# Optimization experiments

Hardware: AMD Instinct MI355X
Metric: run time of the kernel (lower is better)

Reference implementation:

```python
import jax, jax.numpy as jnp
import numpy as np

# NOTE: the original source omits the definitions of QSVT, quantum_lcu_block,
# QuantumSumBlock and KANLayer. We reconstruct the standard math these blocks
# implement in quantum-KAN papers/repos:
#   QSVT(x)            -> vector of Chebyshev polynomials T_1..T_D of the
#                         (squashed) input, the polynomial basis QSVT realizes.
#   quantum_lcu_block  -> linear combination of unitaries: weighted sum of the
#                         QSVT vector normalized by the LCU l1 weight norm.
#   QuantumSumBlock    -> learnable interference sum: mean_k sin(alpha_k * v).
#   KANLayer           -> Chebyshev-KAN layer: spline term (Chebyshev basis
#                         contracted with coeffs) + SiLU base branch + bias.
# Everything is fully vectorized over (B, F) instead of the original per-scalar
# Python loops.

B, F, DEG, C, KBASIS = 16384, 512, 8, 10, 8


def _cheb(x, K):
    """Chebyshev features T_1..T_K of x in (-1, 1): shape x.shape + (K,)."""
    t = jnp.arccos(jnp.clip(x, -1.0, 1.0))
    k = jnp.arange(1, K + 1, dtype=x.dtype)
    return jnp.cos(t[..., None] * k)


def setup_inputs() -> dict:
    key = jax.random.key(0)
    ks = jax.random.split(key, 6)
    return {
        "X": jax.random.normal(ks[0], (B, F), dtype=jnp.float32),
        # nn.Parameter(torch.rand(num_features, degree))
        "lcu_weights": jax.random.uniform(ks[1], (F, DEG), dtype=jnp.float32),
        # one QuantumSumBlock(degree) per feature -> (F, DEG) phases
        "sum_alpha": jax.random.normal(ks[2], (F, DEG), dtype=jnp.float32),
        # KANLayer params
        "kan_coeff": jax.random.normal(ks[3], (C, F, KBASIS), dtype=jnp.float32) * 0.1,
        "kan_base": jax.random.normal(ks[4], (C, F), dtype=jnp.float32) * 0.1,
        "kan_bias": jnp.zeros((C,), dtype=jnp.float32),
    }


def reference(X, lcu_weights, sum_alpha, kan_coeff, kan_base, kan_bias):
    # squash inputs into the open interval (-1, 1) for the Chebyshev/QSVT basis
    x = 0.99 * jnp.tanh(X)                                   # (B, F)
    # QSVT polynomial feature vector per scalar, batched: (B, F, DEG)
    qsvt = _cheb(x, lcu_weights.shape[1])
    # LCU block: weighted combination normalized by l1 norm of weights -> (B, F)
    lcu = jnp.einsum('bfd,fd->bf', qsvt, lcu_weights) / (
        jnp.sum(jnp.abs(lcu_weights), axis=-1) + 1e-8)
    # Quantum sum block: learnable sinusoidal interference sum -> (B, F)
    summed = jnp.mean(jnp.sin(lcu[..., None] * sum_alpha), axis=-1)
    # Chebyshev-KAN layer
    s = 0.99 * jnp.tanh(summed)
    phi = _cheb(s, kan_coeff.shape[2])                       # (B, F, KBASIS)
    logits = (jnp.einsum('bfk,cfk->bc', phi, kan_coeff)
              + jax.nn.silu(summed) @ kan_base.T
              + kan_bias)                                    # (B, C)
    return logits
```

## Files before the change

kernel.cpp:

```cpp
#include <hip/hip_runtime.h>
#include <hip/hip_bf16.h>

#define BATCH 16384
#define NF    512
#define DEG   8
#define NC    10
#define KB    8

#define RB     16
#define PITCH2 520
#define NT     512
#define NWAVES 8

#define CBN (NC * NF * KB)
#define BBN (NC * NF)

#define INV2PI 0.15915494309189535f
#define LOG2E  1.4426950408889634f

typedef __attribute__((ext_vector_type(2))) float v2f;
typedef __attribute__((ext_vector_type(8))) short bfrag;
typedef __attribute__((ext_vector_type(8))) unsigned short us8;
typedef __attribute__((ext_vector_type(4))) float f32x4;

union frag_u { bfrag s; unsigned u[4]; };

__device__ __forceinline__ v2f v2fma(v2f a, v2f b, v2f c) {
    return __builtin_elementwise_fma(a, b, c);
}
__device__ __forceinline__ v2f v2exp(v2f x) {
    v2f a = x * LOG2E;
    v2f r; r.x = __builtin_amdgcn_exp2f(a.x); r.y = __builtin_amdgcn_exp2f(a.y);
    return r;
}
__device__ __forceinline__ v2f v2rcp(v2f x) {
    v2f r; r.x = __builtin_amdgcn_rcpf(x.x); r.y = __builtin_amdgcn_rcpf(x.y);
    return r;
}
__device__ __forceinline__ v2f v2sin2pi(v2f x) {
    v2f r; r.x = __builtin_amdgcn_sinf(x.x); r.y = __builtin_amdgcn_sinf(x.y);
    return r;
}
__device__ __forceinline__ v2f v2tanh99(v2f x) {
    v2f e = v2exp(x + x);
    v2f r = v2rcp(e + 1.0f);
    return v2fma(r, (v2f)(-1.98f), (v2f)(0.99f));
}
__device__ __forceinline__ v2f v2silu(v2f v) {
    v2f e = v2exp(-v);
    v2f r = v2rcp(e + 1.0f);
    return v * r;
}
__device__ __forceinline__ unsigned cvtpk2(float lo, float hi) {
    __hip_bfloat162 h = __float22bfloat162_rn(float2{lo, hi});
    unsigned u;
    __builtin_memcpy(&u, &h, sizeof(u));
    return u;
}
__device__ __forceinline__ float bf2f(unsigned short h) {
    unsigned u = ((unsigned)h) << 16;
    return __builtin_bit_cast(float, u);
}

__global__ __launch_bounds__(256) void prep_kernel(
    const float* __restrict__ coeff, const float* __restrict__ base,
    unsigned short* __restrict__ pk)
{
    const int i = blockIdx.x * 256 + threadIdx.x;
    if (i < CBN)
        pk[i] = (unsigned short)((__builtin_bit_cast(unsigned, coeff[i]) + 0x8000u) >> 16);
    else if (i < CBN + BBN)
        pk[i] = (unsigned short)((__builtin_bit_cast(unsigned, base[i - CBN]) + 0x8000u) >> 16);
}

__global__ __launch_bounds__(NT, 8) void qkan_kernel(
    const float* __restrict__ X,
    const float* __restrict__ lcu_w,
    const float* __restrict__ alpha,
    const unsigned short* __restrict__ pk,
    const float* __restrict__ bias,
    float* __restrict__ out)
{
    __shared__ unsigned short s_mem[RB * PITCH2];
    __shared__ float s_red[NWAVES * RB * 16];

    const int t    = threadIdx.x;
    const int row0 = blockIdx.x * RB;

    {
        const int fA = (t & 255) * 2;
        const int rh = (t >> 8) * 8;

        float wa[2][DEG], aa[2][DEG], den[2];
#pragma unroll
        for (int i = 0; i < 2; ++i) {
            const float4 w0 = *(const float4*)(lcu_w + (fA + i) * DEG);
            const float4 w1 = *(const float4*)(lcu_w + (fA + i) * DEG + 4);
            const float4 a0 = *(const float4*)(alpha + (fA + i) * DEG);
            const float4 a1 = *(const float4*)(alpha + (fA + i) * DEG + 4);
            wa[i][0]=w0.x; wa[i][1]=w0.y; wa[i][2]=w0.z; wa[i][3]=w0.w;
            wa[i][4]=w1.x; wa[i][5]=w1.y; wa[i][6]=w1.z; wa[i][7]=w1.w;
            aa[i][0]=a0.x; aa[i][1]=a0.y; aa[i][2]=a0.z; aa[i][3]=a0.w;
            aa[i][4]=a1.x; aa[i][5]=a1.y; aa[i][6]=a1.z; aa[i][7]=a1.w;
            float d = 1e-8f;
#pragma unroll
            for (int k = 0; k < DEG; ++k) d += fabsf(wa[i][k]);
            den[i] = d;
        }
        v2f W[DEG], A2[DEG];
#pragma unroll
        for (int d = 0; d < DEG; ++d) {
            W[d]  = (v2f){wa[0][d], wa[1][d]};
            A2[d] = (v2f){aa[0][d] * INV2PI, aa[1][d] * INV2PI};
        }
        const v2f rden = (v2f){__builtin_amdgcn_rcpf(den[0]),
                               __builtin_amdgcn_rcpf(den[1])};

#pragma unroll 4
        for (int r8 = 0; r8 < 8; ++r8) {
            const int r = rh + r8;
            const v2f xv = *(const v2f*)(X + (row0 + r) * NF + fA);
            const v2f x  = v2tanh99(xv);
            const v2f x2 = x + x;
            v2f tkm1 = (v2f){1.0f, 1.0f}, tk = x, num = (v2f){0.0f, 0.0f};
#pragma unroll
            for (int d = 0; d < DEG; ++d) {
                num = v2fma(W[d], tk, num);
                v2f tn = v2fma(x2, tk, -tkm1);
                tkm1 = tk; tk = tn;
            }
            const v2f lcu = num * rden;
            v2f ss = (v2f){0.0f, 0.0f};
#pragma unroll
            for (int d = 0; d < DEG; ++d)
                ss += v2sin2pi(lcu * A2[d]);
            const v2f sm = ss * 0.125f;
            *(unsigned*)(&s_mem[r * PITCH2 + fA]) = cvtpk2(sm.x, sm.y);
        }
    }
    __syncthreads();

    const int lane = t & 63;
    const int wave = __builtin_amdgcn_readfirstlane(t >> 6);
    const int n    = lane & 15;
    const int q    = lane >> 4;
    const int ncl  = (n < NC) ? n : (NC - 1);
    const int fw   = wave * 64;

    const unsigned short* cb = pk;
    const unsigned short* bb = pk + CBN;
    const unsigned short* cbase = cb + (ncl * NF + fw) * KB;

    f32x4 acc0 = {0.f, 0.f, 0.f, 0.f};
    f32x4 acc1 = {0.f, 0.f, 0.f, 0.f};

#pragma unroll 4
    for (int kp = 0; kp < 8; ++kp) {
        const bfrag b0 = *(const bfrag*)(cbase + (kp * 8 + q) * KB);
        const bfrag b1 = *(const bfrag*)(cbase + (kp * 8 + 4 + q) * KB);

        const float sA = bf2f(s_mem[n * PITCH2 + fw + kp * 8 + q]);
        const float sB = bf2f(s_mem[n * PITCH2 + fw + kp * 8 + 4 + q]);
        const v2f s  = v2tanh99((v2f){sA, sB});
        const v2f s2 = s + s;
        v2f T[KB];
        {
            v2f tkm1 = (v2f){1.0f, 1.0f}, tk = s;
#pragma unroll
            for (int k = 0; k < KB; ++k) {
                T[k] = tk;
                v2f tn = v2fma(s2, tk, -tkm1);
                tkm1 = tk; tk = tn;
            }
        }
        frag_u fa0, fa1;
#pragma unroll
        for (int i = 0; i < 4; ++i) {
            fa0.u[i] = cvtpk2(T[2 * i].x, T[2 * i + 1].x);
            fa1.u[i] = cvtpk2(T[2 * i].y, T[2 * i + 1].y);
        }
        acc0 = __builtin_amdgcn_mfma_f32_16x16x32_bf16(fa0.s, b0, acc0, 0, 0, 0);
        acc1 = __builtin_amdgcn_mfma_f32_16x16x32_bf16(fa1.s, b1, acc1, 0, 0, 0);
    }

#pragma unroll
    for (int kt2 = 0; kt2 < 2; ++kt2) {
        const bfrag b = *(const bfrag*)(bb + ncl * NF + fw + kt2 * 32 + q * 8);
        const us8 sv = *(const us8*)(&s_mem[n * PITCH2 + fw + kt2 * 32 + q * 8]);
        v2f vv[4];
#pragma unroll
        for (int g = 0; g < 4; ++g)
            vv[g] = (v2f){bf2f(sv[2 * g]), bf2f(sv[2 * g + 1])};
        frag_u fa;
#pragma unroll
        for (int g = 0; g < 4; ++g) {
            const v2f sl = v2silu(vv[g]);
            fa.u[g] = cvtpk2(sl.x, sl.y);
        }
        if (kt2 & 1)
            acc1 = __builtin_amdgcn_mfma_f32_16x16x32_bf16(fa.s, b, acc1, 0, 0, 0);
        else
            acc0 = __builtin_amdgcn_mfma_f32_16x16x32_bf16(fa.s, b, acc0, 0, 0, 0);
    }

    const f32x4 acc = acc0 + acc1;
#pragma unroll
    for (int i = 0; i < 4; ++i)
        s_red[wave * (RB * 16) + (q * 4 + i) * 16 + n] = acc[i];
    __syncthreads();

    if (t < RB * NC) {
        const int r = t / NC;
        const int c = t - r * NC;
        float v = bias[c];
#pragma unroll
        for (int w = 0; w < NWAVES; ++w)
            v += s_red[w * (RB * 16) + r * 16 + c];
        out[(row0 + r) * NC + c] = v;
    }
}

extern "C" void kernel_launch(void* const* d_in, const int* in_sizes, int n_in,
                              void* d_out, int out_size, void* d_ws, size_t ws_size,
                              hipStream_t stream) {
    const float* X      = (const float*)d_in[0];
    const float* lcu_w  = (const float*)d_in[1];
    const float* alpha  = (const float*)d_in[2];
    const float* coeff  = (const float*)d_in[3];
    const float* base   = (const float*)d_in[4];
    const float* bias   = (const float*)d_in[5];
    float* out = (float*)d_out;
    unsigned short* pk = (unsigned short*)d_ws;

    prep_kernel<<<(CBN + BBN + 255) / 256, 256, 0, stream>>>(coeff, base, pk);
    qkan_kernel<<<BATCH / RB, NT, 0, stream>>>(X, lcu_w, alpha, pk, bias, out);
}
```

Before: 101.6 us.

## Compute tanh and SiLU in the first stage and halve block threads

After: 100.9 us. About the same (-0.7%).

```diff
diff --git a/kernel.cpp b/kernel.cpp
--- a/kernel.cpp
+++ b/kernel.cpp
@@ -9,8 +9,8 @@
 
 #define RB     16
 #define PITCH2 520
-#define NT     512
-#define NWAVES 8
+#define NT     256
+#define NWAVES 4
 
 #define CBN (NC * NF * KB)
 #define BBN (NC * NF)
@@ -23,7 +23,8 @@
 typedef __attribute__((ext_vector_type(8))) unsigned short us8;
 typedef __attribute__((ext_vector_type(4))) float f32x4;
 
-union frag_u { bfrag s; unsigned u[4]; };
+union frag_u  { bfrag s; unsigned u[4]; };
+union frag_u2 { us8 v; bfrag s; };
 
 __device__ __forceinline__ v2f v2fma(v2f a, v2f b, v2f c) {
     return __builtin_elementwise_fma(a, b, c);
@@ -45,11 +46,6 @@
     v2f e = v2exp(x + x);
     v2f r = v2rcp(e + 1.0f);
     return v2fma(r, (v2f)(-1.98f), (v2f)(0.99f));
-}
-__device__ __forceinline__ v2f v2silu(v2f v) {
-    v2f e = v2exp(-v);
-    v2f r = v2rcp(e + 1.0f);
-    return v * r;
 }
 __device__ __forceinline__ unsigned cvtpk2(float lo, float hi) {
     __hip_bfloat162 h = __float22bfloat162_rn(float2{lo, hi});
@@ -73,7 +69,7 @@
         pk[i] = (unsigned short)((__builtin_bit_cast(unsigned, base[i - CBN]) + 0x8000u) >> 16);
 }
 
-__global__ __launch_bounds__(NT, 8) void qkan_kernel(
+__global__ __launch_bounds__(NT, 4) void qkan_kernel(
     const float* __restrict__ X,
     const float* __restrict__ lcu_w,
     const float* __restrict__ alpha,
@@ -81,15 +77,15 @@
     const float* __restrict__ bias,
     float* __restrict__ out)
 {
-    __shared__ unsigned short s_mem[RB * PITCH2];
+    __shared__ unsigned short s_s[RB * PITCH2];
+    __shared__ unsigned short s_l[RB * PITCH2];
     __shared__ float s_red[NWAVES * RB * 16];
 
     const int t    = threadIdx.x;
     const int row0 = blockIdx.x * RB;
 
     {
-        const int fA = (t & 255) * 2;
-        const int rh = (t >> 8) * 8;
+        const int fA = t * 2;
 
         float wa[2][DEG], aa[2][DEG], den[2];
 #pragma unroll
@@ -117,8 +113,7 @@
                                __builtin_amdgcn_rcpf(den[1])};
 
 #pragma unroll 4
-        for (int r8 = 0; r8 < 8; ++r8) {
-            const int r = rh + r8;
+        for (int r = 0; r < RB; ++r) {
             const v2f xv = *(const v2f*)(X + (row0 + r) * NF + fA);
             const v2f x  = v2tanh99(xv);
             const v2f x2 = x + x;
@@ -135,7 +130,14 @@
             for (int d = 0; d < DEG; ++d)
                 ss += v2sin2pi(lcu * A2[d]);
             const v2f sm = ss * 0.125f;
-            *(unsigned*)(&s_mem[r * PITCH2 + fA]) = cvtpk2(sm.x, sm.y);
+
+            const v2f E  = v2exp(sm);
+            const v2f s  = v2fma(v2rcp(v2fma(E, E, (v2f)(1.0f))),
+                                 (v2f)(-1.98f), (v2f)(0.99f));
+            const v2f si = sm * E * v2rcp(E + 1.0f);
+
+            *(unsigned*)(&s_s[r * PITCH2 + fA]) = cvtpk2(s.x, s.y);
+            *(unsigned*)(&s_l[r * PITCH2 + fA]) = cvtpk2(si.x, si.y);
         }
     }
     __syncthreads();
@@ -145,7 +147,7 @@
     const int n    = lane & 15;
     const int q    = lane >> 4;
     const int ncl  = (n < NC) ? n : (NC - 1);
-    const int fw   = wave * 64;
+    const int fw   = wave * 128;
 
     const unsigned short* cb = pk;
     const unsigned short* bb = pk + CBN;
@@ -155,13 +157,13 @@
     f32x4 acc1 = {0.f, 0.f, 0.f, 0.f};
 
 #pragma unroll 4
-    for (int kp = 0; kp < 8; ++kp) {
+    for (int kp = 0; kp < 16; ++kp) {
         const bfrag b0 = *(const bfrag*)(cbase + (kp * 8 + q) * KB);
         const bfrag b1 = *(const bfrag*)(cbase + (kp * 8 + 4 + q) * KB);
 
-        const float sA = bf2f(s_mem[n * PITCH2 + fw + kp * 8 + q]);
-        const float sB = bf2f(s_mem[n * PITCH2 + fw + kp * 8 + 4 + q]);
-        const v2f s  = v2tanh99((v2f){sA, sB});
+        const float sA = bf2f(s_s[n * PITCH2 + fw + kp * 8 + q]);
+        const float sB = bf2f(s_s[n * PITCH2 + fw + kp * 8 + 4 + q]);
+        const v2f s  = (v2f){sA, sB};
         const v2f s2 = s + s;
         v2f T[KB];
         {
@@ -184,19 +186,10 @@
     }
 
 #pragma unroll
-    for (int kt2 = 0; kt2 < 2; ++kt2) {
+    for (int kt2 = 0; kt2 < 4; ++kt2) {
         const bfrag b = *(const bfrag*)(bb + ncl * NF + fw + kt2 * 32 + q * 8);
-        const us8 sv = *(const us8*)(&s_mem[n * PITCH2 + fw + kt2 * 32 + q * 8]);
-        v2f vv[4];
-#pragma unroll
-        for (int g = 0; g < 4; ++g)
-            vv[g] = (v2f){bf2f(sv[2 * g]), bf2f(sv[2 * g + 1])};
-        frag_u fa;
-#pragma unroll
-        for (int g = 0; g < 4; ++g) {
-            const v2f sl = v2silu(vv[g]);
-            fa.u[g] = cvtpk2(sl.x, sl.y);
-        }
+        frag_u2 fa;
+        fa.v = *(const us8*)(&s_l[n * PITCH2 + fw + kt2 * 32 + q * 8]);
         if (kt2 & 1)
             acc1 = __builtin_amdgcn_mfma_f32_16x16x32_bf16(fa.s, b, acc1, 0, 0, 0);
         else
```
